# Performance work log

Hardware: AMD Instinct MI355X
Metric: run time of the kernel (lower is better)

## Reference

```python
import jax, jax.numpy as jnp
import numpy as np

INPUT_DIM = 512
HIDDEN_DIM = 256
REP_DIM = 256
SCORE_HIDDEN = 128


def setup_inputs() -> dict:
    key = jax.random.key(0)
    ks = jax.random.split(key, 12)
    def rn(k, shape, scale=None):
        s = scale if scale is not None else 1.0 / np.sqrt(shape[0])
        return jax.random.normal(k, shape, dtype=jnp.float32) * s
    return {
        "feat_x": jax.random.normal(ks[0], (512, INPUT_DIM), dtype=jnp.float32),
        "feat_pos": jax.random.normal(ks[1], (512, INPUT_DIM), dtype=jnp.float32),
        "feat_neg": jax.random.normal(ks[2], (512, INPUT_DIM), dtype=jnp.float32),
        # g: Linear(input,hidden) -> GELU -> Linear(hidden,rep); stored as x @ W
        "g_w1": rn(ks[3], (INPUT_DIM, HIDDEN_DIM)),
        "g_b1": jnp.zeros((HIDDEN_DIM,), jnp.float32),
        "g_w2": rn(ks[4], (HIDDEN_DIM, REP_DIM)),
        "g_b2": jnp.zeros((REP_DIM,), jnp.float32),
        # out_proj: Linear(rep, input, bias=False)
        "out_w": rn(ks[5], (REP_DIM, INPUT_DIM)),
        # score_net: Linear(3*rep+1, score_hidden) -> GELU -> Linear(score_hidden, 1)
        "s_w1": rn(ks[6], (3 * REP_DIM + 1, SCORE_HIDDEN)),
        "s_b1": jnp.zeros((SCORE_HIDDEN,), jnp.float32),
        "s_w2": rn(ks[7], (SCORE_HIDDEN, 1)),
        "s_b2": jnp.zeros((1,), jnp.float32),
    }


def _gelu(x):
    return jax.nn.gelu(x, approximate=False)  # torch nn.GELU default = exact erf


def _g(x, g_w1, g_b1, g_w2, g_b2):
    return _gelu(x @ g_w1 + g_b1) @ g_w2 + g_b2


def _set_operator(feat_x, feat_set, params):
    g_w1, g_b1, g_w2, g_b2, out_w, s_w1, s_b1, s_w2, s_b2 = params
    x_rep = _g(feat_x, g_w1, g_b1, g_w2, g_b2)   # (n, r)
    y_rep = _g(feat_set, g_w1, g_b1, g_w2, g_b2)  # (m, r)
    n, r = x_rep.shape
    m = y_rep.shape[0]
    x_exp = jnp.broadcast_to(x_rep[:, None, :], (n, m, r))
    y_exp = jnp.broadcast_to(y_rep[None, :, :], (n, m, r))
    delta = y_exp - x_exp                                   # (n, m, r)
    delta_norm = jnp.linalg.norm(delta, axis=-1, keepdims=True)
    score_in = jnp.concatenate([x_exp, y_exp, delta, delta_norm], axis=-1)  # (n, m, 3r+1)
    logits = (_gelu(score_in @ s_w1 + s_b1) @ s_w2 + s_b2)[..., 0]          # (n, m)
    weights = jax.nn.softmax(logits, axis=1)
    set_update_rep = jnp.einsum("nm,nmr->nr", weights, delta)
    return set_update_rep @ out_w


def reference(feat_x, feat_pos, feat_neg, g_w1, g_b1, g_w2, g_b2, out_w, s_w1, s_b1, s_w2, s_b2):
    params = (g_w1, g_b1, g_w2, g_b2, out_w, s_w1, s_b1, s_w2, s_b2)
    s_pos = _set_operator(feat_x, feat_pos, params)
    s_neg = _set_operator(feat_x, feat_neg, params)  # mask_self_neg=False
    return s_pos - s_neg
```

## Files before the change

kernel.cpp:

```cpp
#include <hip/hip_runtime.h>
#include <math.h>

#define NN 512
#define IN 512
#define HD 256
#define RD 256
#define SH 128

__device__ __forceinline__ float gelu_fast(float x){
    const float z  = x * 0.70710678118654752f;
    const float az = fabsf(z);
    const float t  = __builtin_amdgcn_rcpf(fmaf(0.3275911f, az, 1.0f));
    float p = fmaf(1.061405429f, t, -1.453152027f);
    p = fmaf(p, t, 1.421413741f);
    p = fmaf(p, t, -0.284496736f);
    p = fmaf(p, t, 0.254829592f);
    p = p * t;
    const float e = __builtin_amdgcn_exp2f(z * z * -1.4426950408889634f);
    const float E = p * e;
    const float one_plus_erf = (x >= 0.0f) ? (2.0f - E) : E;
    return 0.5f * x * one_plus_erf;
}

__device__ __forceinline__ float gelu2(float u){
    const float az = fabsf(u);
    const float tt = __builtin_amdgcn_rcpf(fmaf(0.3326725f, az, 1.0f));
    const float P  = fmaf(fmaf(0.7478556f, tt, -0.0958798f), tt, 0.3480242f) * tt;
    const float e2 = __builtin_amdgcn_exp2f(u * u * -0.72134752044448170f);
    const float Eq = P * e2;
    const float ope = (u >= 0.0f) ? (2.0f - Eq) : Eq;
    return u * ope;
}

__global__ __launch_bounds__(512) void k_rep(
    const float* __restrict__ fx, const float* __restrict__ fp, const float* __restrict__ fn,
    const float* __restrict__ w1, const float* __restrict__ b1,
    const float* __restrict__ w2, const float* __restrict__ b2,
    const float* __restrict__ s_w1,
    float* __restrict__ r_x, float* __restrict__ r_p, float* __restrict__ r_n,
    float* __restrict__ rT_p, float* __restrict__ rT_n,
    float* __restrict__ A_x, float* __restrict__ BT_p, float* __restrict__ BT_n,
    float* __restrict__ nx2, float* __restrict__ np2, float* __restrict__ nn2)
{
    __shared__ float xs[4][IN];
    __shared__ float ps[8][4][HD];
    __shared__ float hs[4][HD];
    __shared__ float rloc[4][RD];
    __shared__ float ab4[4][SH];
    const int t = threadIdx.x;
    const int mat = blockIdx.x >> 7;
    const int row0 = (blockIdx.x & 127) << 2;
    const float* src = (mat==0) ? fx : (mat==1) ? fp : fn;

    {
        const int j = t >> 7, c4 = (t & 127) << 2;
        *(float4*)&xs[j][c4] = *(const float4*)&src[(row0+j)*IN + c4];
    }
    __syncthreads();

    const int cg = t & 63, s = t >> 6;
    const int c0 = cg << 2;

    {
        float4 acc[4];
        #pragma unroll
        for (int j=0;j<4;j++) acc[j] = make_float4(0.f,0.f,0.f,0.f);
        const float* wp = w1 + (s*64)*HD + c0;
        #pragma unroll 8
        for (int ii=0; ii<64; ii++){
            float4 w = *(const float4*)wp; wp += HD;
            const int i = s*64 + ii;
            #pragma unroll
            for (int j=0;j<4;j++){
                const float xv = xs[j][i];
                acc[j].x = fmaf(xv, w.x, acc[j].x);
                acc[j].y = fmaf(xv, w.y, acc[j].y);
                acc[j].z = fmaf(xv, w.z, acc[j].z);
                acc[j].w = fmaf(xv, w.w, acc[j].w);
            }
        }
        #pragma unroll
        for (int j=0;j<4;j++) *(float4*)&ps[s][j][c0] = acc[j];
    }
    __syncthreads();

    #pragma unroll
    for (int rep=0; rep<2; rep++){
        const int idx = rep*512 + t;
        const int j = idx >> 8, c = idx & 255;
        float v = b1[c];
        #pragma unroll
        for (int ss=0; ss<8; ss++) v += ps[ss][j][c];
        hs[j][c] = gelu_fast(v);
    }
    __syncthreads();

    {
        float4 acc[4];
        #pragma unroll
        for (int j=0;j<4;j++) acc[j] = make_float4(0.f,0.f,0.f,0.f);
        const float* wp = w2 + (s*32)*RD + c0;
        #pragma unroll 8
        for (int ii=0; ii<32; ii++){
            float4 w = *(const float4*)wp; wp += RD;
            const int i = s*32 + ii;
            #pragma unroll
            for (int j=0;j<4;j++){
                const float xv = hs[j][i];
                acc[j].x = fmaf(xv, w.x, acc[j].x);
                acc[j].y = fmaf(xv, w.y, acc[j].y);
                acc[j].z = fmaf(xv, w.z, acc[j].z);
                acc[j].w = fmaf(xv, w.w, acc[j].w);
            }
        }
        #pragma unroll
        for (int j=0;j<4;j++) *(float4*)&ps[s][j][c0] = acc[j];
    }
    __syncthreads();

    float* rout = (mat==0) ? r_x : (mat==1) ? r_p : r_n;
    #pragma unroll
    for (int rep=0; rep<2; rep++){
        const int idx = rep*512 + t;
        const int j = idx >> 8, c = idx & 255;
        float v = b2[c];
        #pragma unroll
        for (int ss=0; ss<8; ss++) v += ps[ss][j][c];
        rloc[j][c] = v;
        rout[(row0+j)*RD + c] = v;
    }
    __syncthreads();

    if (t < 256){
        const int w = t >> 6, l = t & 63;
        float v = 0.f;
        #pragma unroll
        for (int q=0;q<4;q++){ const float e = rloc[w][l + 64*q]; v = fmaf(e,e,v); }
        #pragma unroll
        for (int off=32; off>=1; off>>=1) v += __shfl_xor(v, off);
        if (l==0){
            float* nrm = (mat==0) ? nx2 : (mat==1) ? np2 : nn2;
            nrm[row0 + w] = v;
        }
    }
    if (mat && t < 256){
        float* rT = (mat==1) ? rT_p : rT_n;
        float4 q = make_float4(rloc[0][t], rloc[1][t], rloc[2][t], rloc[3][t]);
        *(float4*)&rT[t*NN + row0] = q;
    }

    {
        const int cg2 = t & 31, s2 = t >> 5;
        const int cc0 = cg2 << 2;
        const float sgn = (mat==0) ? -1.0f : 1.0f;
        const int base1 = (mat==0) ? 0 : 256;
        const float* p1 = s_w1 + (base1 + s2*16)*SH + cc0;
        const float* p3 = s_w1 + (512   + s2*16)*SH + cc0;
        float4 a[4];
        #pragma unroll
        for (int j=0;j<4;j++) a[j] = make_float4(0.f,0.f,0.f,0.f);
        #pragma unroll 8
        for (int ii=0; ii<16; ii++){
            float4 wa = *(const float4*)p1; p1 += SH;
            float4 wd = *(const float4*)p3; p3 += SH;
            float4 w;
            w.x = fmaf(sgn, wd.x, wa.x);
            w.y = fmaf(sgn, wd.y, wa.y);
            w.z = fmaf(sgn, wd.z, wa.z);
            w.w = fmaf(sgn, wd.w, wa.w);
            const int i = s2*16 + ii;
            #pragma unroll
            for (int j=0;j<4;j++){
                const float xv = rloc[j][i];
                a[j].x = fmaf(xv, w.x, a[j].x);
                a[j].y = fmaf(xv, w.y, a[j].y);
                a[j].z = fmaf(xv, w.z, a[j].z);
                a[j].w = fmaf(xv, w.w, a[j].w);
            }
        }
        float* psf = &ps[0][0][0];
        #pragma unroll
        for (int j=0;j<4;j++) *(float4*)&psf[(s2*4 + j)*SH + cc0] = a[j];
    }
    __syncthreads();

    {
        const float* psf = &ps[0][0][0];
        const int j = t >> 7, c = t & 127;
        float v = 0.f;
        #pragma unroll
        for (int ss=0; ss<16; ss++) v += psf[(ss*4 + j)*SH + c];
        if (mat==0) A_x[(row0+j)*SH + c] = v;
        else        ab4[j][c] = v;
    }
    __syncthreads();
    if (mat && t < 128){
        float* BT = (mat==1) ? BT_p : BT_n;
        float4 q = make_float4(ab4[0][t], ab4[1][t], ab4[2][t], ab4[3][t]);
        *(float4*)&BT[t*NN + row0] = q;
    }
}

__global__ __launch_bounds__(256) void k_sd(
    const float* __restrict__ r_x, const float* __restrict__ rT_p, const float* __restrict__ rT_n,
    const float* __restrict__ A_x, const float* __restrict__ BT_p, const float* __restrict__ BT_n,
    const float* __restrict__ r_p, const float* __restrict__ r_n,
    const float* __restrict__ nx2, const float* __restrict__ np2, const float* __restrict__ nn2,
    const float* __restrict__ s_w1, const float* __restrict__ s_b1,
    const float* __restrict__ s_w2,
    float* __restrict__ psum, float* __restrict__ Spart)
{
    __shared__ float4 xs4[RD];
    __shared__ float4 cmbA[SH];
    __shared__ float2 cmbW[SH];
    __shared__ float pda[4][64];
    __shared__ float pdb[4][64];
    __shared__ float pdc[4][64];
    __shared__ float pdd[4][64];
    __shared__ float ny2v[64];
    __shared__ float4 evb4[64];
    const int t = threadIdx.x;
    const int set = blockIdx.x >> 10;
    const int rem = blockIdx.x & 1023;
    const int n0 = (rem >> 3) << 2;
    const int mt = rem & 7;
    const int mbase = mt << 6;
    const int tm = t & 63, kh = t >> 6;
    const int m = mbase + tm;
    const float* yT = set ? rT_n : rT_p;
    const float* BT = set ? BT_n : BT_p;

    xs4[t] = make_float4(r_x[n0*RD + t],       r_x[(n0+1)*RD + t],
                         r_x[(n0+2)*RD + t],   r_x[(n0+3)*RD + t]);
    if (t < SH){
        const float b1v = s_b1[t];
        cmbA[t] = make_float4(A_x[n0*SH + t] + b1v,     A_x[(n0+1)*SH + t] + b1v,
                              A_x[(n0+2)*SH + t] + b1v, A_x[(n0+3)*SH + t] + b1v);
        cmbW[t] = make_float2(s_w1[768*SH + t], 0.5f * s_w2[t]);
    }
    if (t < 64) ny2v[t] = (set ? nn2 : np2)[mbase + t];
    const float nxa = nx2[n0];
    const float nxb = nx2[n0 + 1];
    const float nxc = nx2[n0 + 2];
    const float nxd = nx2[n0 + 3];
    __syncthreads();

    float d0=0.f, d1=0.f, d2=0.f, d3=0.f;
    {
        const float* yp = yT + (kh << 6)*NN + m;
        #pragma unroll 8
        for (int rr=0; rr<64; rr++){
            const float y = yp[rr*NN];
            const float4 xv = xs4[(kh << 6) + rr];
            d0 = fmaf(xv.x, y, d0);
            d1 = fmaf(xv.y, y, d1);
            d2 = fmaf(xv.z, y, d2);
            d3 = fmaf(xv.w, y, d3);
        }
    }
    pda[kh][tm] = d0; pdb[kh][tm] = d1; pdc[kh][tm] = d2; pdd[kh][tm] = d3;
    __syncthreads();
    d0 = pda[0][tm] + pda[1][tm] + pda[2][tm] + pda[3][tm];
    d1 = pdb[0][tm] + pdb[1][tm] + pdb[2][tm] + pdb[3][tm];
    d2 = pdc[0][tm] + pdc[1][tm] + pdc[2][tm] + pdc[3][tm];
    d3 = pdd[0][tm] + pdd[1][tm] + pdd[2][tm] + pdd[3][tm];
    const float nyc = ny2v[tm];
    const float dn0 = sqrtf(fmaxf(fmaf(-2.f, d0, nxa + nyc), 0.f));
    const float dn1 = sqrtf(fmaxf(fmaf(-2.f, d1, nxb + nyc), 0.f));
    const float dn2 = sqrtf(fmaxf(fmaf(-2.f, d2, nxc + nyc), 0.f));
    const float dn3 = sqrtf(fmaxf(fmaf(-2.f, d3, nxd + nyc), 0.f));

    float a0=0.f, a1=0.f, a2=0.f, a3=0.f;
    {
        const float* bp = BT + (kh << 5)*NN + m;
        #pragma unroll 4
        for (int kk=0; kk<32; kk++){
            const float b = bp[kk*NN];
            const float4 cA = cmbA[(kh << 5) + kk];
            const float2 w  = cmbW[(kh << 5) + kk];
            a0 = fmaf(w.y, gelu2(fmaf(dn0, w.x, cA.x + b)), a0);
            a1 = fmaf(w.y, gelu2(fmaf(dn1, w.x, cA.y + b)), a1);
            a2 = fmaf(w.y, gelu2(fmaf(dn2, w.x, cA.z + b)), a2);
            a3 = fmaf(w.y, gelu2(fmaf(dn3, w.x, cA.w + b)), a3);
        }
    }
    __syncthreads();
    pda[kh][tm] = a0; pdb[kh][tm] = a1; pdc[kh][tm] = a2; pdd[kh][tm] = a3;
    __syncthreads();
    if (kh == 0){
        const float L2E = 1.4426950408889634f;
        const float l0 = pda[0][tm]+pda[1][tm]+pda[2][tm]+pda[3][tm];
        const float l1 = pdb[0][tm]+pdb[1][tm]+pdb[2][tm]+pdb[3][tm];
        const float l2 = pdc[0][tm]+pdc[1][tm]+pdc[2][tm]+pdc[3][tm];
        const float l3 = pdd[0][tm]+pdd[1][tm]+pdd[2][tm]+pdd[3][tm];
        const float ev0 = __builtin_amdgcn_exp2f(l0 * L2E);
        const float ev1 = __builtin_amdgcn_exp2f(l1 * L2E);
        const float ev2 = __builtin_amdgcn_exp2f(l2 * L2E);
        const float ev3 = __builtin_amdgcn_exp2f(l3 * L2E);
        evb4[tm] = make_float4(ev0, ev1, ev2, ev3);
        float v0 = ev0, v1 = ev1, v2 = ev2, v3 = ev3;
        #pragma unroll
        for (int off=32; off>=1; off>>=1){
            v0 += __shfl_xor(v0, off); v1 += __shfl_xor(v1, off);
            v2 += __shfl_xor(v2, off); v3 += __shfl_xor(v3, off);
        }
        if (tm == 0){
            float* Sp = Spart + (set*8 + mt)*NN + n0;
            Sp[0] = v0; Sp[1] = v1; Sp[2] = v2; Sp[3] = v3;
        }
    }
    __syncthreads();

    {
        const float* ry = (set ? r_n : r_p) + mbase*RD + t;
        float e0 = 0.f, e1 = 0.f, e2 = 0.f, e3 = 0.f;
        #pragma unroll 8
        for (int mm=0; mm<64; mm++){
            const float rv = ry[mm*RD];
            const float4 w = evb4[mm];
            e0 = fmaf(w.x, rv, e0);
            e1 = fmaf(w.y, rv, e1);
            e2 = fmaf(w.z, rv, e2);
            e3 = fmaf(w.w, rv, e3);
        }
        float* P = psum + ((set*8 + mt)*NN + n0)*RD;
        P[t]        = e0;
        P[RD + t]   = e1;
        P[2*RD + t] = e2;
        P[3*RD + t] = e3;
    }
}

__global__ __launch_bounds__(256) void k_fin(
    const float* __restrict__ psum, const float* __restrict__ Spart,
    const float* __restrict__ out_w, float* __restrict__ out)
{
    __shared__ float dv[2][RD];
    const int t = threadIdx.x;
    const int np = blockIdx.x >> 2, ct = blockIdx.x & 3;
    const int n0 = np << 1;
    const int cb = ct << 7;

    #pragma unroll
    for (int rep=0; rep<2; rep++){
        const int idx = rep*256 + t;
        const int j = idx >> 8, c = idx & 255;
        const int n = n0 + j;
        float Sp = 0.f, Sn = 0.f;
        #pragma unroll
        for (int q=0;q<8;q++){
            Sp += Spart[q*NN + n];
            Sn += Spart[(8+q)*NN + n];
        }
        float vp = 0.f, vn = 0.f;
        #pragma unroll
        for (int q=0;q<8;q++){
            vp += psum[(q*NN + n)*RD + c];
            vn += psum[((8+q)*NN + n)*RD + c];
        }
        dv[j][c] = vp * (1.0f/Sp) - vn * (1.0f/Sn);
    }
    __syncthreads();

    {
        const int j = t >> 7, cc = t & 127;
        const int col = cb + cc;
        float o = 0.f;
        const float* wo = out_w + col;
        #pragma unroll 8
        for (int r=0; r<RD; r++){ o = fmaf(dv[j][r], *wo, o); wo += IN; }
        out[(n0+j)*IN + col] = o;
    }
}

extern "C" void kernel_launch(void* const* d_in, const int* in_sizes, int n_in,
                              void* d_out, int out_size, void* d_ws, size_t ws_size,
                              hipStream_t stream)
{
    const float* fx  = (const float*)d_in[0];
    const float* fp  = (const float*)d_in[1];
    const float* fn  = (const float*)d_in[2];
    const float* gw1 = (const float*)d_in[3];
    const float* gb1 = (const float*)d_in[4];
    const float* gw2 = (const float*)d_in[5];
    const float* gb2 = (const float*)d_in[6];
    const float* ow  = (const float*)d_in[7];
    const float* sw1 = (const float*)d_in[8];
    const float* sb1 = (const float*)d_in[9];
    const float* sw2 = (const float*)d_in[10];
    float* out = (float*)d_out;

    float* ws   = (float*)d_ws;
    float* r_x  = ws;
    float* r_p  = r_x  + 131072;
    float* r_n  = r_p  + 131072;
    float* rT_p = r_n  + 131072;
    float* rT_n = rT_p + 131072;
    float* A_x  = rT_n + 131072;
    float* BT_p = A_x  + 65536;
    float* BT_n = BT_p + 65536;
    float* Spar = BT_n + 65536;
    float* nx2  = Spar + 8192;
    float* np2  = nx2  + 512;
    float* nn2  = np2  + 512;
    float* psum = nn2  + 512;

    hipLaunchKernelGGL(k_rep, dim3(384), dim3(512), 0, stream,
                       fx, fp, fn, gw1, gb1, gw2, gb2, sw1,
                       r_x, r_p, r_n, rT_p, rT_n, A_x, BT_p, BT_n,
                       nx2, np2, nn2);
    hipLaunchKernelGGL(k_sd, dim3(2048), dim3(256), 0, stream,
                       r_x, rT_p, rT_n, A_x, BT_p, BT_n, r_p, r_n,
                       nx2, np2, nn2, sw1, sb1, sw2, psum, Spar);
    hipLaunchKernelGGL(k_fin, dim3(1024), dim3(256), 0, stream,
                       psum, Spar, ow, out);
}
```

Before: 155.1 us.

## Assign each wavefront one query row in score MLP instead of splitting hidden dim

The score-MLP stage is repartitioned so each of the four wavefronts owns one of the four x rows and loops over all 128 hidden units, rather than each wave covering a quarter of the hidden units for all four rows. This removes one cross-wave shared-memory reduction and its barriers for the logits. Softmax exponentials and row sums are then computed per wave in parallel. The GELU evaluation is also simplified to a single fma with the sign folded in via |u|. In exchange each thread reloads the B column 128 times instead of 32, and the per-row constants are packed into a padded float4 table.

```diff
diff --git a/kernel.cpp b/kernel.cpp
--- a/kernel.cpp
+++ b/kernel.cpp
@@ -22,14 +22,12 @@
     return 0.5f * x * one_plus_erf;
 }
 
-__device__ __forceinline__ float gelu2(float u){
-    const float az = fabsf(u);
-    const float tt = __builtin_amdgcn_rcpf(fmaf(0.3326725f, az, 1.0f));
+__device__ __forceinline__ float gelu2b(float u){
+    const float au = fabsf(u);
+    const float tt = __builtin_amdgcn_rcpf(fmaf(0.3326725f, au, 1.0f));
     const float P  = fmaf(fmaf(0.7478556f, tt, -0.0958798f), tt, 0.3480242f) * tt;
     const float e2 = __builtin_amdgcn_exp2f(u * u * -0.72134752044448170f);
-    const float Eq = P * e2;
-    const float ope = (u >= 0.0f) ? (2.0f - Eq) : Eq;
-    return u * ope;
+    return fmaf(-au, P * e2, u + au);
 }
 
 __global__ __launch_bounds__(512) void k_rep(
@@ -211,13 +209,9 @@
     float* __restrict__ psum, float* __restrict__ Spart)
 {
     __shared__ float4 xs4[RD];
-    __shared__ float4 cmbA[SH];
-    __shared__ float2 cmbW[SH];
-    __shared__ float pda[4][64];
-    __shared__ float pdb[4][64];
-    __shared__ float pdc[4][64];
-    __shared__ float pdd[4][64];
-    __shared__ float ny2v[64];
+    __shared__ float4 cmb4[4][SH];
+    __shared__ float  pd[4][4][64];
+    __shared__ float  ny2v[64];
     __shared__ float4 evb4[64];
     const int t = threadIdx.x;
     const int set = blockIdx.x >> 10;
@@ -230,23 +224,24 @@
     const float* yT = set ? rT_n : rT_p;
     const float* BT = set ? BT_n : BT_p;
 
+    const float nxv = nx2[n0 + kh];
+
     xs4[t] = make_float4(r_x[n0*RD + t],       r_x[(n0+1)*RD + t],
                          r_x[(n0+2)*RD + t],   r_x[(n0+3)*RD + t]);
     if (t < SH){
         const float b1v = s_b1[t];
-        cmbA[t] = make_float4(A_x[n0*SH + t] + b1v,     A_x[(n0+1)*SH + t] + b1v,
-                              A_x[(n0+2)*SH + t] + b1v, A_x[(n0+3)*SH + t] + b1v);
-        cmbW[t] = make_float2(s_w1[768*SH + t], 0.5f * s_w2[t]);
+        const float wn  = s_w1[768*SH + t];
+        const float w2h = 0.5f * s_w2[t];
+        cmb4[0][t] = make_float4(A_x[ n0     *SH + t] + b1v, wn, w2h, 0.f);
+        cmb4[1][t] = make_float4(A_x[(n0+1)*SH + t] + b1v, wn, w2h, 0.f);
+        cmb4[2][t] = make_float4(A_x[(n0+2)*SH + t] + b1v, wn, w2h, 0.f);
+        cmb4[3][t] = make_float4(A_x[(n0+3)*SH + t] + b1v, wn, w2h, 0.f);
     }
     if (t < 64) ny2v[t] = (set ? nn2 : np2)[mbase + t];
-    const float nxa = nx2[n0];
-    const float nxb = nx2[n0 + 1];
-    const float nxc = nx2[n0 + 2];
-    const float nxd = nx2[n0 + 3];
-    __syncthreads();
-
-    float d0=0.f, d1=0.f, d2=0.f, d3=0.f;
-    {
+    __syncthreads();
+
+    {
+        float d0=0.f, d1=0.f, d2=0.f, d3=0.f;
         const float* yp = yT + (kh << 6)*NN + m;
         #pragma unroll 8
         for (int rr=0; rr<64; rr++){
@@ -257,57 +252,35 @@
             d2 = fmaf(xv.z, y, d2);
             d3 = fmaf(xv.w, y, d3);
         }
-    }
-    pda[kh][tm] = d0; pdb[kh][tm] = d1; pdc[kh][tm] = d2; pdd[kh][tm] = d3;
-    __syncthreads();
-    d0 = pda[0][tm] + pda[1][tm] + pda[2][tm] + pda[3][tm];
-    d1 = pdb[0][tm] + pdb[1][tm] + pdb[2][tm] + pdb[3][tm];
-    d2 = pdc[0][tm] + pdc[1][tm] + pdc[2][tm] + pdc[3][tm];
-    d3 = pdd[0][tm] + pdd[1][tm] + pdd[2][tm] + pdd[3][tm];
-    const float nyc = ny2v[tm];
-    const float dn0 = sqrtf(fmaxf(fmaf(-2.f, d0, nxa + nyc), 0.f));
-    const float dn1 = sqrtf(fmaxf(fmaf(-2.f, d1, nxb + nyc), 0.f));
-    const float dn2 = sqrtf(fmaxf(fmaf(-2.f, d2, nxc + nyc), 0.f));
-    const float dn3 = sqrtf(fmaxf(fmaf(-2.f, d3, nxd + nyc), 0.f));
-
-    float a0=0.f, a1=0.f, a2=0.f, a3=0.f;
-    {
-        const float* bp = BT + (kh << 5)*NN + m;
+        pd[0][kh][tm] = d0; pd[1][kh][tm] = d1;
+        pd[2][kh][tm] = d2; pd[3][kh][tm] = d3;
+    }
+    __syncthreads();
+
+    const float dsum = pd[kh][0][tm] + pd[kh][1][tm] + pd[kh][2][tm] + pd[kh][3][tm];
+    const float dn = sqrtf(fmaxf(fmaf(-2.f, dsum, nxv + ny2v[tm]), 0.f));
+
+    float acc = 0.f;
+    {
+        const float* bp = BT + m;
+        const float4* cp = cmb4[kh];
         #pragma unroll 4
-        for (int kk=0; kk<32; kk++){
-            const float b = bp[kk*NN];
-            const float4 cA = cmbA[(kh << 5) + kk];
-            const float2 w  = cmbW[(kh << 5) + kk];
-            a0 = fmaf(w.y, gelu2(fmaf(dn0, w.x, cA.x + b)), a0);
-            a1 = fmaf(w.y, gelu2(fmaf(dn1, w.x, cA.y + b)), a1);
-            a2 = fmaf(w.y, gelu2(fmaf(dn2, w.x, cA.z + b)), a2);
-            a3 = fmaf(w.y, gelu2(fmaf(dn3, w.x, cA.w + b)), a3);
-        }
-    }
-    __syncthreads();
-    pda[kh][tm] = a0; pdb[kh][tm] = a1; pdc[kh][tm] = a2; pdd[kh][tm] = a3;
-    __syncthreads();
-    if (kh == 0){
+        for (int k=0; k<SH; k++){
+            const float  B  = bp[k*NN];
+            const float4 cw = cp[k];
+            const float  u  = fmaf(dn, cw.y, cw.x + B);
+            acc = fmaf(cw.z, gelu2b(u), acc);
+        }
+    }
+
+    {
         const float L2E = 1.4426950408889634f;
-        const float l0 = pda[0][tm]+pda[1][tm]+pda[2][tm]+pda[3][tm];
-        const float l1 = pdb[0][tm]+pdb[1][tm]+pdb[2][tm]+pdb[3][tm];
-        const float l2 = pdc[0][tm]+pdc[1][tm]+pdc[2][tm]+pdc[3][tm];
-        const float l3 = pdd[0][tm]+pdd[1][tm]+pdd[2][tm]+pdd[3][tm];
-        const float ev0 = __builtin_amdgcn_exp2f(l0 * L2E);
-        const float ev1 = __builtin_amdgcn_exp2f(l1 * L2E);
-        const float ev2 = __builtin_amdgcn_exp2f(l2 * L2E);
-        const float ev3 = __builtin_amdgcn_exp2f(l3 * L2E);
-        evb4[tm] = make_float4(ev0, ev1, ev2, ev3);
-        float v0 = ev0, v1 = ev1, v2 = ev2, v3 = ev3;
-        #pragma unroll
-        for (int off=32; off>=1; off>>=1){
-            v0 += __shfl_xor(v0, off); v1 += __shfl_xor(v1, off);
-            v2 += __shfl_xor(v2, off); v3 += __shfl_xor(v3, off);
-        }
-        if (tm == 0){
-            float* Sp = Spart + (set*8 + mt)*NN + n0;
-            Sp[0] = v0; Sp[1] = v1; Sp[2] = v2; Sp[3] = v3;
-        }
+        const float ev = __builtin_amdgcn_exp2f(acc * L2E);
+        ((float*)evb4)[tm*4 + kh] = ev;
+        float v = ev;
+        #pragma unroll
+        for (int off=32; off>=1; off>>=1) v += __shfl_xor(v, off);
+        if (tm == 0) Spart[(set*8 + mt)*NN + n0 + kh] = v;
     }
     __syncthreads();
 
```

Result: no change. 155.7 us (+0.4%).
